# Kernel tuning notes

Measured on AMD Instinct MI355X. Metric: run time of the kernel, lower is better.

The kernel has to match this reference:

```python
import jax, jax.numpy as jnp
import numpy as np

B, S, D = 2, 2048, 1024
H, DH = 16, 64
EPS = 1e-5

def setup_inputs() -> dict:
    key = jax.random.key(0)
    ks = jax.random.split(key, 8)
    s = 0.02
    return {
        "x": jax.random.normal(ks[0], (B, S, D), dtype=jnp.float32),
        "ln_gamma": jnp.ones((D,), jnp.float32),
        "ln_beta": jnp.zeros((D,), jnp.float32),
        "wq": jax.random.normal(ks[1], (D, H * DH), jnp.float32) * s,
        "bq": jnp.zeros((H * DH,), jnp.float32),
        "wk": jax.random.normal(ks[2], (D, H * DH), jnp.float32) * s,
        "bk": jnp.zeros((H * DH,), jnp.float32),
        "wv": jax.random.normal(ks[3], (D, H * DH), jnp.float32) * s,
        "bv": jnp.zeros((H * DH,), jnp.float32),
        "wo": jax.random.normal(ks[4], (H * DH, D), jnp.float32) * s,
        "bo": jnp.zeros((D,), jnp.float32),
    }

def reference(x, ln_gamma, ln_beta, wq, bq, wk, bk, wv, bv, wo, bo):
    # Pre-LayerNorm over d_model
    mu = jnp.mean(x, axis=-1, keepdims=True)
    var = jnp.var(x, axis=-1, keepdims=True)
    xn = (x - mu) * jax.lax.rsqrt(var + EPS) * ln_gamma + ln_beta

    b, s, _ = xn.shape
    q = (xn @ wq + bq).reshape(b, s, H, DH)
    k = (xn @ wk + bk).reshape(b, s, H, DH)
    v = (xn @ wv + bv).reshape(b, s, H, DH)

    scale = jnp.sqrt(jnp.float32(DH))
    scores = jnp.einsum('bihd,bjhd->bhij', q, k) / scale  # [b,h,s,s]
    att = jax.nn.softmax(scores, axis=-1)
    out = jnp.einsum('bhij,bjhd->bihd', att, v).reshape(b, s, H * DH)
    return out @ wo + bo
```

## Files before the change

### kernel.cpp

```cpp
#include <hip/hip_runtime.h>
#include <math.h>

#define SEQ   2048
#define DM    1024
#define NHEAD 16
#define HD    64
#define NTOK  4096
#define EPS   1e-5f
#define SCALE_C 0.18033688f

typedef __attribute__((ext_vector_type(8))) short v8s;
typedef __attribute__((ext_vector_type(4))) short v4s;
typedef __attribute__((ext_vector_type(4))) float v4f;
typedef unsigned short ushort_t;

#define GLOAD16(g, l) __builtin_amdgcn_global_load_lds( \
    (const __attribute__((address_space(1))) unsigned int*)(g), \
    (__attribute__((address_space(3))) unsigned int*)(l), 16, 0, 0)

#if defined(__has_builtin)
#if __has_builtin(__builtin_amdgcn_mfma_f32_16x16x16_bf16)
#define MFMA16(va, vb, vc) __builtin_amdgcn_mfma_f32_16x16x16_bf16(va, vb, vc, 0, 0, 0)
#elif __has_builtin(__builtin_amdgcn_mfma_f32_16x16x16bf16_1k)
#define MFMA16(va, vb, vc) __builtin_amdgcn_mfma_f32_16x16x16bf16_1k(va, vb, vc, 0, 0, 0)
#endif
#endif
#ifndef MFMA16
__device__ __forceinline__ v4f mfma16_asm(v4s a, v4s b, v4f c) {
  asm volatile("s_nop 2\n\tv_mfma_f32_16x16x16_bf16 %0, %1, %2, %0\n\ts_nop 4"
               : "+v"(c) : "v"(a), "v"(b));
  return c;
}
#define MFMA16(va, vb, vc) mfma16_asm(va, vb, vc)
#endif

__device__ __forceinline__ unsigned short f2bf(float f) {
  union { float f; unsigned u; } v; v.f = f;
  unsigned r = v.u + 0x7FFFu + ((v.u >> 16) & 1u);
  return (unsigned short)(r >> 16);
}

__device__ __forceinline__ unsigned pack2_bf16(float a, float b) {
  union { float f; unsigned u; } ua, ub;
  ua.f = a; ub.f = b;
  return __builtin_amdgcn_perm(ub.u + 0x8000u, ua.u + 0x8000u, 0x07060302u);
}

__global__ __launch_bounds__(256) void ln_kernel(
    const float* __restrict__ x, const float* __restrict__ g,
    const float* __restrict__ be, ushort_t* __restrict__ y) {
  const int row = blockIdx.x;
  const int t = threadIdx.x;
  const float4 v = ((const float4*)(x + (size_t)row * DM))[t];
  float s  = v.x + v.y + v.z + v.w;
  float ss = v.x*v.x + v.y*v.y + v.z*v.z + v.w*v.w;
  #pragma unroll
  for (int off = 32; off > 0; off >>= 1) {
    s  += __shfl_down(s,  off, 64);
    ss += __shfl_down(ss, off, 64);
  }
  __shared__ float red[8];
  __shared__ float mu_s, rs_s;
  const int wid = t >> 6, lane = t & 63;
  if (lane == 0) { red[wid] = s; red[4 + wid] = ss; }
  __syncthreads();
  if (t == 0) {
    const float S  = red[0] + red[1] + red[2] + red[3];
    const float SS = red[4] + red[5] + red[6] + red[7];
    const float mu  = S * (1.0f / DM);
    const float var = SS * (1.0f / DM) - mu * mu;
    mu_s = mu; rs_s = rsqrtf(var + EPS);
  }
  __syncthreads();
  const float mu = mu_s, r = rs_s;
  const float4 gv = ((const float4*)g)[t];
  const float4 bv = ((const float4*)be)[t];
  ushort4 o;
  o.x = f2bf((v.x - mu) * r * gv.x + bv.x);
  o.y = f2bf((v.y - mu) * r * gv.y + bv.y);
  o.z = f2bf((v.z - mu) * r * gv.z + bv.z);
  o.w = f2bf((v.w - mu) * r * gv.w + bv.w);
  *(ushort4*)(y + (size_t)row * DM + t * 4) = o;
}

__global__ __launch_bounds__(256) void wt_kernel(
    const float* __restrict__ w0, const float* __restrict__ w1,
    const float* __restrict__ w2, const float* __restrict__ w3,
    ushort_t* __restrict__ o0, ushort_t* __restrict__ o1,
    ushort_t* __restrict__ o2, ushort_t* __restrict__ o3) {
  const int z = blockIdx.z;
  const float* w = (z==0) ? w0 : (z==1) ? w1 : (z==2) ? w2 : w3;
  ushort_t* o    = (z==0) ? o0 : (z==1) ? o1 : (z==2) ? o2 : o3;
  __shared__ float tile[64][65];
  const int t = threadIdx.x;
  const int n0 = blockIdx.x * 64, k0 = blockIdx.y * 64;
  const int r = t >> 4, c4 = (t & 15) * 4;
  #pragma unroll
  for (int i = 0; i < 4; ++i) {
    const float4 v = *(const float4*)(w + (size_t)(k0 + r + i*16) * DM + n0 + c4);
    tile[r + i*16][c4 + 0] = v.x;
    tile[r + i*16][c4 + 1] = v.y;
    tile[r + i*16][c4 + 2] = v.z;
    tile[r + i*16][c4 + 3] = v.w;
  }
  __syncthreads();
  #pragma unroll
  for (int i = 0; i < 4; ++i) {
    const int n = r + i*16;
    ushort4 o4;
    o4.x = f2bf(tile[c4 + 0][n]);
    o4.y = f2bf(tile[c4 + 1][n]);
    o4.z = f2bf(tile[c4 + 2][n]);
    o4.w = f2bf(tile[c4 + 3][n]);
    *(ushort4*)(o + (size_t)(n0 + n) * DM + k0 + c4) = o4;
  }
}

__device__ __forceinline__ void gemm_main(ushort_t* lsa, ushort_t* lsb,
    const ushort_t* A, const ushort_t* WT, int m0, int n0, v4f acc[4][4]) {
  const int tid = threadIdx.x;
  const int wid = tid >> 6, lane = tid & 63;
  const int mh = (wid & 1) << 6, nh = (wid >> 1) << 6;
  const int r16 = lane & 15, quad = lane >> 4;
  const int srow = lane >> 2, sch = lane & 3;
  for (int k0 = 0; k0 < DM; k0 += 32) {
    __syncthreads();
    #pragma unroll
    for (int j = 0; j < 2; ++j) {
      const int o = wid * 2 + j;
      GLOAD16(A  + (size_t)(m0 + o*16 + srow) * DM + k0 + sch*8, lsa + o*512);
      GLOAD16(WT + (size_t)(n0 + o*16 + srow) * DM + k0 + sch*8, lsb + o*512);
    }
    __syncthreads();
    v8s af[4], bfr[4];
    #pragma unroll
    for (int i = 0; i < 4; ++i) {
      af[i]  = *(const v8s*)(lsa + (mh + i*16 + r16)*32 + quad*8);
      bfr[i] = *(const v8s*)(lsb + (nh + i*16 + r16)*32 + quad*8);
    }
    #pragma unroll
    for (int i = 0; i < 4; ++i)
      #pragma unroll
      for (int j = 0; j < 4; ++j)
        acc[i][j] = __builtin_amdgcn_mfma_f32_16x16x32_bf16(af[i], bfr[j], acc[i][j], 0, 0, 0);
  }
}

__global__ __launch_bounds__(256, 2) void gemm_qkv(const ushort_t* __restrict__ xn,
    const ushort_t* __restrict__ wtq, const ushort_t* __restrict__ wtk, const ushort_t* __restrict__ wtv,
    const float* __restrict__ bq, const float* __restrict__ bk, const float* __restrict__ bv,
    ushort_t* __restrict__ qo, ushort_t* __restrict__ ko, ushort_t* __restrict__ vto) {
  __shared__ ushort_t lsa[128*32];
  __shared__ ushort_t lsb[128*32];
  const int z = blockIdx.z;
  const ushort_t* WT = (z == 0) ? wtq : (z == 1) ? wtk : wtv;
  const float* bias  = (z == 0) ? bq  : (z == 1) ? bk  : bv;
  const int m0 = blockIdx.y * 128, n0 = blockIdx.x * 128;
  v4f acc[4][4];
  #pragma unroll
  for (int i = 0; i < 4; ++i)
    #pragma unroll
    for (int j = 0; j < 4; ++j) acc[i][j] = (v4f){0.f, 0.f, 0.f, 0.f};
  gemm_main(lsa, lsb, xn, WT, m0, n0, acc);
  const int tid = threadIdx.x, wid = tid >> 6, lane = tid & 63;
  const int mh = (wid & 1) << 6, nh = (wid >> 1) << 6;
  const int r16 = lane & 15, quad = lane >> 4;
  if (z < 2) {
    ushort_t* out = (z == 0) ? qo : ko;
    const float sc = (z == 0) ? SCALE_C : 1.0f;
    #pragma unroll
    for (int bn = 0; bn < 4; ++bn) {
      const int col = n0 + nh + bn*16 + r16;
      const float bb = bias[col];
      #pragma unroll
      for (int am = 0; am < 4; ++am) {
        const int tb = m0 + mh + am*16 + quad*4;
        #pragma unroll
        for (int r = 0; r < 4; ++r)
          out[(size_t)(tb + r) * DM + col] = f2bf((acc[am][bn][r] + bb) * sc);
      }
    }
  } else {
    #pragma unroll
    for (int bn = 0; bn < 4; ++bn) {
      const int col = n0 + nh + bn*16 + r16;
      const float bb = bias[col];
      const int h = col >> 6, d = col & 63;
      #pragma unroll
      for (int am = 0; am < 4; ++am) {
        const int tb = m0 + mh + am*16 + quad*4;
        const int b = tb >> 11, t = tb & 2047;
        const int bh = b * NHEAD + h;
        ushort4 o4;
        o4.x = f2bf(acc[am][bn][0] + bb);
        o4.y = f2bf(acc[am][bn][1] + bb);
        o4.z = f2bf(acc[am][bn][2] + bb);
        o4.w = f2bf(acc[am][bn][3] + bb);
        const size_t idx = (size_t)bh * 131072 + (size_t)(t >> 6) * 4096 +
                           (size_t)((((t >> 4) & 3) * 4) + (d >> 4)) * 256 +
                           ((t >> 2) & 3) * 64 + (d & 15) * 4;
        *(ushort4*)(vto + idx) = o4;
      }
    }
  }
}

__global__ __launch_bounds__(256, 2) void gemm_out(const ushort_t* __restrict__ A,
    const ushort_t* __restrict__ WT, const float* __restrict__ bias,
    float* __restrict__ out) {
  __shared__ ushort_t lsa[128*32];
  __shared__ ushort_t lsb[128*32];
  const int m0 = blockIdx.y * 128, n0 = blockIdx.x * 128;
  v4f acc[4][4];
  #pragma unroll
  for (int i = 0; i < 4; ++i)
    #pragma unroll
    for (int j = 0; j < 4; ++j) acc[i][j] = (v4f){0.f, 0.f, 0.f, 0.f};
  gemm_main(lsa, lsb, A, WT, m0, n0, acc);
  const int tid = threadIdx.x, wid = tid >> 6, lane = tid & 63;
  const int mh = (wid & 1) << 6, nh = (wid >> 1) << 6;
  const int r16 = lane & 15, quad = lane >> 4;
  #pragma unroll
  for (int bn = 0; bn < 4; ++bn) {
    const int col = n0 + nh + bn*16 + r16;
    const float bb = bias[col];
    #pragma unroll
    for (int am = 0; am < 4; ++am) {
      const int tb = m0 + mh + am*16 + quad*4;
      #pragma unroll
      for (int r = 0; r < 4; ++r)
        out[(size_t)(tb + r) * DM + col] = acc[am][bn][r] + bb;
    }
  }
}

#define OHALF ((size_t)32 * 2048 * 64)
#define LHALF (32 * 2048)
template<int SPLIT>
__global__ __launch_bounds__(256, 8) void attn_kernel(
    const ushort_t* __restrict__ Q, const ushort_t* __restrict__ K,
    const ushort_t* __restrict__ Vt, ushort_t* __restrict__ O,
    float* __restrict__ Opart, float* __restrict__ lpart) {
  __shared__ ushort_t kbuf[8*512];
  __shared__ ushort_t vbuf[16*256];
  const int tid = threadIdx.x, wid = tid >> 6, lane = tid & 63;
  const int r16 = lane & 15, quad = lane >> 4;
  const int q0 = blockIdx.x * 64, bh = blockIdx.y;
  const int half = SPLIT ? blockIdx.z : 0;
  const int b = bh >> 4, h = bh & 15;
  const ushort_t* gQ = Q + (size_t)b * SEQ * DM + h * HD;
  const ushort_t* gK = K + (size_t)b * SEQ * DM + h * HD;
  const ushort_t* gV = Vt + (size_t)bh * 131072;

  const int qtok = q0 + wid * 16 + r16;
  const v8s qf0 = *(const v8s*)(gQ + (size_t)qtok * DM + quad * 8);
  const v8s qf1 = *(const v8s*)(gQ + (size_t)qtok * DM + 32 + quad * 8);
  v4f acco[4];
  #pragma unroll
  for (int i = 0; i < 4; ++i) acco[i] = (v4f){0.f, 0.f, 0.f, 0.f};
  float lrun = 0.f;

  const int NIT = SPLIT ? (SEQ / 128) : (SEQ / 64);
  const int kt0 = half * NIT;
  for (int it = 0; it < NIT; ++it) {
    const int kt = kt0 + it;
    const int k0 = kt * 64;
    __syncthreads();
    #pragma unroll
    for (int j = 0; j < 2; ++j) {
      const int o = wid * 2 + j;
      GLOAD16(gK + (size_t)(k0 + (o >> 1) * 16 + r16) * DM + (o & 1) * 32 + quad * 8,
              kbuf + o * 512);
    }
    #pragma unroll
    for (int j = 0; j < 2; ++j) {
      const int o = wid * 2 + j;
      GLOAD16(gV + (size_t)kt * 4096 + o * 512 + lane * 8, vbuf + o * 512);
    }
    __syncthreads();

    v4f sacc[4];
    #pragma unroll
    for (int g = 0; g < 4; ++g) sacc[g] = (v4f){0.f, 0.f, 0.f, 0.f};
    #pragma unroll
    for (int g = 0; g < 4; ++g) {
      const v8s ka0 = *(const v8s*)(kbuf + (g*2 + 0) * 512 + lane * 8);
      const v8s ka1 = *(const v8s*)(kbuf + (g*2 + 1) * 512 + lane * 8);
      sacc[g] = __builtin_amdgcn_mfma_f32_16x16x32_bf16(ka0, qf0, sacc[g], 0, 0, 0);
      sacc[g] = __builtin_amdgcn_mfma_f32_16x16x32_bf16(ka1, qf1, sacc[g], 0, 0, 0);
    }

    float ls = 0.f;
    v4s pfrag[4];
    #pragma unroll
    for (int g = 0; g < 4; ++g) {
      float e0 = __builtin_amdgcn_exp2f(sacc[g][0]);
      float e1 = __builtin_amdgcn_exp2f(sacc[g][1]);
      float e2 = __builtin_amdgcn_exp2f(sacc[g][2]);
      float e3 = __builtin_amdgcn_exp2f(sacc[g][3]);
      ls += (e0 + e1) + (e2 + e3);
      union { v4s s; uint2 u; } pk;
      pk.u.x = pack2_bf16(e0, e1);
      pk.u.y = pack2_bf16(e2, e3);
      pfrag[g] = pk.s;
    }
    ls += __shfl_xor(ls, 16, 64);
    ls += __shfl_xor(ls, 32, 64);
    lrun += ls;

    #pragma unroll
    for (int dg = 0; dg < 4; ++dg) {
      #pragma unroll
      for (int g = 0; g < 4; ++g) {
        const v4s vf = *(const v4s*)(vbuf + (g*4 + dg) * 256 + quad * 64 + r16 * 4);
        acco[dg] = MFMA16(vf, pfrag[g], acco[dg]);
      }
    }
  }

  if (SPLIT) {
    float* Op = Opart + half * OHALF + ((size_t)bh * SEQ + qtok) * 64;
    #pragma unroll
    for (int dg = 0; dg < 4; ++dg)
      *(v4f*)(Op + dg*16 + quad*4) = acco[dg];
    if (quad == 0) lpart[half * LHALF + bh * SEQ + qtok] = lrun;
  } else {
    const float inv = 1.f / lrun;
    ushort_t* gO = O + (size_t)b * SEQ * DM + h * HD;
    #pragma unroll
    for (int dg = 0; dg < 4; ++dg) {
      ushort4 o4;
      o4.x = f2bf(acco[dg][0] * inv);
      o4.y = f2bf(acco[dg][1] * inv);
      o4.z = f2bf(acco[dg][2] * inv);
      o4.w = f2bf(acco[dg][3] * inv);
      *(ushort4*)(gO + (size_t)qtok * DM + dg*16 + quad*4) = o4;
    }
  }
}

__global__ __launch_bounds__(256) void combine_kernel(
    const float* __restrict__ Opart, const float* __restrict__ lpart,
    ushort_t* __restrict__ ob) {
  const int tok = blockIdx.x;
  const int b = tok >> 11, t = tok & 2047;
  const int dm0 = threadIdx.x * 4;
  const int h = dm0 >> 6, d = dm0 & 63;
  const int bh = b * NHEAD + h;
  const size_t idx = ((size_t)bh * SEQ + t) * 64 + d;
  const float4 a = *(const float4*)(Opart + idx);
  const float4 c = *(const float4*)(Opart + OHALF + idx);
  const float l = lpart[bh * SEQ + t] + lpart[LHALF + bh * SEQ + t];
  const float inv = 1.f / l;
  ushort4 o4;
  o4.x = f2bf((a.x + c.x) * inv);
  o4.y = f2bf((a.y + c.y) * inv);
  o4.z = f2bf((a.z + c.z) * inv);
  o4.w = f2bf((a.w + c.w) * inv);
  *(ushort4*)(ob + (size_t)tok * DM + dm0) = o4;
}

extern "C" void kernel_launch(void* const* d_in, const int* in_sizes, int n_in,
                              void* d_out, int out_size, void* d_ws, size_t ws_size,
                              hipStream_t stream) {
  const float* x     = (const float*)d_in[0];
  const float* gamma = (const float*)d_in[1];
  const float* beta  = (const float*)d_in[2];
  const float* wq    = (const float*)d_in[3];
  const float* bq    = (const float*)d_in[4];
  const float* wk    = (const float*)d_in[5];
  const float* bk    = (const float*)d_in[6];
  const float* wv    = (const float*)d_in[7];
  const float* bv    = (const float*)d_in[8];
  const float* wo    = (const float*)d_in[9];
  const float* bo    = (const float*)d_in[10];
  float* out = (float*)d_out;

  unsigned char* w8 = (unsigned char*)d_ws;
  const size_t MB = 1024 * 1024;
  ushort_t* xn  = (ushort_t*)(w8 + 0 * MB);
  ushort_t* qb  = (ushort_t*)(w8 + 8 * MB);
  ushort_t* kb  = (ushort_t*)(w8 + 16 * MB);
  ushort_t* vt  = (ushort_t*)(w8 + 24 * MB);
  ushort_t* wtq = (ushort_t*)(w8 + 32 * MB);
  ushort_t* wtk = (ushort_t*)(w8 + 34 * MB);
  ushort_t* wtv = (ushort_t*)(w8 + 36 * MB);
  ushort_t* wto = (ushort_t*)(w8 + 38 * MB);
  float* Opart  = (float*)(w8 + 40 * MB);
  float* lpart  = (float*)(w8 + 72 * MB);
  ushort_t* ob  = xn;

  ln_kernel<<<dim3(NTOK), dim3(256), 0, stream>>>(x, gamma, beta, xn);
  wt_kernel<<<dim3(16, 16, 4), dim3(256), 0, stream>>>(wq, wk, wv, wo, wtq, wtk, wtv, wto);
  gemm_qkv<<<dim3(8, 32, 3), dim3(256), 0, stream>>>(xn, wtq, wtk, wtv, bq, bk, bv, qb, kb, vt);
  if (ws_size >= 73 * MB) {
    attn_kernel<1><<<dim3(SEQ / 64, 2 * NHEAD, 2), dim3(256), 0, stream>>>(
        qb, kb, vt, nullptr, Opart, lpart);
    combine_kernel<<<dim3(NTOK), dim3(256), 0, stream>>>(Opart, lpart, ob);
  } else {
    attn_kernel<0><<<dim3(SEQ / 64, 2 * NHEAD, 1), dim3(256), 0, stream>>>(
        qb, kb, vt, ob, nullptr, nullptr);
  }
  gemm_out<<<dim3(8, 32, 1), dim3(256), 0, stream>>>(ob, wto, bo, out);
}
```

Baseline: 217.7 us.

## Double-buffer K/V tiles in attention and merge layernorm with weight transpose

The attention kernel now keeps two LDS buffers for K and V and issues the global-to-LDS loads for the next tile before computing on the current one. This drops one barrier per iteration and lets memory traffic overlap the MFMA work. The layernorm and weight-transpose kernels are also merged into one launch, with block index choosing the role, which saves a launch and lets the two run side by side. The costs are doubled LDS per attention block, which may lower occupancy under the 8-block launch bound, and one extra redundant tile load on the last iteration.

Result: no change. 218.5 us (+0.4%).

```diff
diff --git a/kernel.cpp b/kernel.cpp
--- a/kernel.cpp
+++ b/kernel.cpp
@@ -46,73 +46,73 @@
   return __builtin_amdgcn_perm(ub.u + 0x8000u, ua.u + 0x8000u, 0x07060302u);
 }
 
-__global__ __launch_bounds__(256) void ln_kernel(
+__global__ __launch_bounds__(256) void prep_kernel(
     const float* __restrict__ x, const float* __restrict__ g,
-    const float* __restrict__ be, ushort_t* __restrict__ y) {
-  const int row = blockIdx.x;
-  const int t = threadIdx.x;
-  const float4 v = ((const float4*)(x + (size_t)row * DM))[t];
-  float s  = v.x + v.y + v.z + v.w;
-  float ss = v.x*v.x + v.y*v.y + v.z*v.z + v.w*v.w;
-  #pragma unroll
-  for (int off = 32; off > 0; off >>= 1) {
-    s  += __shfl_down(s,  off, 64);
-    ss += __shfl_down(ss, off, 64);
-  }
-  __shared__ float red[8];
-  __shared__ float mu_s, rs_s;
-  const int wid = t >> 6, lane = t & 63;
-  if (lane == 0) { red[wid] = s; red[4 + wid] = ss; }
-  __syncthreads();
-  if (t == 0) {
-    const float S  = red[0] + red[1] + red[2] + red[3];
-    const float SS = red[4] + red[5] + red[6] + red[7];
-    const float mu  = S * (1.0f / DM);
-    const float var = SS * (1.0f / DM) - mu * mu;
-    mu_s = mu; rs_s = rsqrtf(var + EPS);
-  }
-  __syncthreads();
-  const float mu = mu_s, r = rs_s;
-  const float4 gv = ((const float4*)g)[t];
-  const float4 bv = ((const float4*)be)[t];
-  ushort4 o;
-  o.x = f2bf((v.x - mu) * r * gv.x + bv.x);
-  o.y = f2bf((v.y - mu) * r * gv.y + bv.y);
-  o.z = f2bf((v.z - mu) * r * gv.z + bv.z);
-  o.w = f2bf((v.w - mu) * r * gv.w + bv.w);
-  *(ushort4*)(y + (size_t)row * DM + t * 4) = o;
-}
-
-__global__ __launch_bounds__(256) void wt_kernel(
+    const float* __restrict__ be, ushort_t* __restrict__ y,
     const float* __restrict__ w0, const float* __restrict__ w1,
     const float* __restrict__ w2, const float* __restrict__ w3,
     ushort_t* __restrict__ o0, ushort_t* __restrict__ o1,
     ushort_t* __restrict__ o2, ushort_t* __restrict__ o3) {
-  const int z = blockIdx.z;
-  const float* w = (z==0) ? w0 : (z==1) ? w1 : (z==2) ? w2 : w3;
-  ushort_t* o    = (z==0) ? o0 : (z==1) ? o1 : (z==2) ? o2 : o3;
+  __shared__ float red[8];
+  __shared__ float mu_s, rs_s;
   __shared__ float tile[64][65];
   const int t = threadIdx.x;
-  const int n0 = blockIdx.x * 64, k0 = blockIdx.y * 64;
-  const int r = t >> 4, c4 = (t & 15) * 4;
-  #pragma unroll
-  for (int i = 0; i < 4; ++i) {
-    const float4 v = *(const float4*)(w + (size_t)(k0 + r + i*16) * DM + n0 + c4);
-    tile[r + i*16][c4 + 0] = v.x;
-    tile[r + i*16][c4 + 1] = v.y;
-    tile[r + i*16][c4 + 2] = v.z;
-    tile[r + i*16][c4 + 3] = v.w;
-  }
-  __syncthreads();
-  #pragma unroll
-  for (int i = 0; i < 4; ++i) {
-    const int n = r + i*16;
-    ushort4 o4;
-    o4.x = f2bf(tile[c4 + 0][n]);
-    o4.y = f2bf(tile[c4 + 1][n]);
-    o4.z = f2bf(tile[c4 + 2][n]);
-    o4.w = f2bf(tile[c4 + 3][n]);
-    *(ushort4*)(o + (size_t)(n0 + n) * DM + k0 + c4) = o4;
+  if (blockIdx.x < NTOK) {
+    const int row = blockIdx.x;
+    const float4 v = ((const float4*)(x + (size_t)row * DM))[t];
+    float s  = v.x + v.y + v.z + v.w;
+    float ss = v.x*v.x + v.y*v.y + v.z*v.z + v.w*v.w;
+    #pragma unroll
+    for (int off = 32; off > 0; off >>= 1) {
+      s  += __shfl_down(s,  off, 64);
+      ss += __shfl_down(ss, off, 64);
+    }
+    const int wid = t >> 6, lane = t & 63;
+    if (lane == 0) { red[wid] = s; red[4 + wid] = ss; }
+    __syncthreads();
+    if (t == 0) {
+      const float S  = red[0] + red[1] + red[2] + red[3];
+      const float SS = red[4] + red[5] + red[6] + red[7];
+      const float mu  = S * (1.0f / DM);
+      const float var = SS * (1.0f / DM) - mu * mu;
+      mu_s = mu; rs_s = rsqrtf(var + EPS);
+    }
+    __syncthreads();
+    const float mu = mu_s, r = rs_s;
+    const float4 gv = ((const float4*)g)[t];
+    const float4 bv = ((const float4*)be)[t];
+    ushort4 o;
+    o.x = f2bf((v.x - mu) * r * gv.x + bv.x);
+    o.y = f2bf((v.y - mu) * r * gv.y + bv.y);
+    o.z = f2bf((v.z - mu) * r * gv.z + bv.z);
+    o.w = f2bf((v.w - mu) * r * gv.w + bv.w);
+    *(ushort4*)(y + (size_t)row * DM + t * 4) = o;
+  } else {
+    const int i = blockIdx.x - NTOK;
+    const int z = i >> 8;
+    const float* w = (z==0) ? w0 : (z==1) ? w1 : (z==2) ? w2 : w3;
+    ushort_t* o    = (z==0) ? o0 : (z==1) ? o1 : (z==2) ? o2 : o3;
+    const int n0 = (i & 15) * 64, k0 = ((i >> 4) & 15) * 64;
+    const int r = t >> 4, c4 = (t & 15) * 4;
+    #pragma unroll
+    for (int ii = 0; ii < 4; ++ii) {
+      const float4 v = *(const float4*)(w + (size_t)(k0 + r + ii*16) * DM + n0 + c4);
+      tile[r + ii*16][c4 + 0] = v.x;
+      tile[r + ii*16][c4 + 1] = v.y;
+      tile[r + ii*16][c4 + 2] = v.z;
+      tile[r + ii*16][c4 + 3] = v.w;
+    }
+    __syncthreads();
+    #pragma unroll
+    for (int ii = 0; ii < 4; ++ii) {
+      const int n = r + ii*16;
+      ushort4 o4;
+      o4.x = f2bf(tile[c4 + 0][n]);
+      o4.y = f2bf(tile[c4 + 1][n]);
+      o4.z = f2bf(tile[c4 + 2][n]);
+      o4.w = f2bf(tile[c4 + 3][n]);
+      *(ushort4*)(o + (size_t)(n0 + n) * DM + k0 + c4) = o4;
+    }
   }
 }
 
@@ -241,8 +241,8 @@
     const ushort_t* __restrict__ Q, const ushort_t* __restrict__ K,
     const ushort_t* __restrict__ Vt, ushort_t* __restrict__ O,
     float* __restrict__ Opart, float* __restrict__ lpart) {
-  __shared__ ushort_t kbuf[8*512];
-  __shared__ ushort_t vbuf[16*256];
+  __shared__ ushort_t kbuf[2][8*512];
+  __shared__ ushort_t vbuf[2][16*256];
   const int tid = threadIdx.x, wid = tid >> 6, lane = tid & 63;
   const int r16 = lane & 15, quad = lane >> 4;
   const int q0 = blockIdx.x * 64, bh = blockIdx.y;
@@ -262,30 +262,36 @@
 
   const int NIT = SPLIT ? (SEQ / 128) : (SEQ / 64);
   const int kt0 = half * NIT;
-  for (int it = 0; it < NIT; ++it) {
-    const int kt = kt0 + it;
+
+  auto stage = [&](int bs, int kt) {
     const int k0 = kt * 64;
-    __syncthreads();
     #pragma unroll
     for (int j = 0; j < 2; ++j) {
       const int o = wid * 2 + j;
       GLOAD16(gK + (size_t)(k0 + (o >> 1) * 16 + r16) * DM + (o & 1) * 32 + quad * 8,
-              kbuf + o * 512);
+              kbuf[bs] + o * 512);
     }
     #pragma unroll
     for (int j = 0; j < 2; ++j) {
       const int o = wid * 2 + j;
-      GLOAD16(gV + (size_t)kt * 4096 + o * 512 + lane * 8, vbuf + o * 512);
-    }
-    __syncthreads();
+      GLOAD16(gV + (size_t)kt * 4096 + o * 512 + lane * 8, vbuf[bs] + o * 512);
+    }
+  };
+
+  stage(0, kt0);
+  __syncthreads();
+
+  for (int it = 0; it < NIT; ++it) {
+    const int cur = it & 1;
+    stage(cur ^ 1, kt0 + ((it + 1 == NIT) ? 0 : it + 1));
 
     v4f sacc[4];
     #pragma unroll
     for (int g = 0; g < 4; ++g) sacc[g] = (v4f){0.f, 0.f, 0.f, 0.f};
     #pragma unroll
     for (int g = 0; g < 4; ++g) {
-      const v8s ka0 = *(const v8s*)(kbuf + (g*2 + 0) * 512 + lane * 8);
-      const v8s ka1 = *(const v8s*)(kbuf + (g*2 + 1) * 512 + lane * 8);
+      const v8s ka0 = *(const v8s*)(kbuf[cur] + (g*2 + 0) * 512 + lane * 8);
+      const v8s ka1 = *(const v8s*)(kbuf[cur] + (g*2 + 1) * 512 + lane * 8);
       sacc[g] = __builtin_amdgcn_mfma_f32_16x16x32_bf16(ka0, qf0, sacc[g], 0, 0, 0);
       sacc[g] = __builtin_amdgcn_mfma_f32_16x16x32_bf16(ka1, qf1, sacc[g], 0, 0, 0);
     }
@@ -312,10 +318,12 @@
     for (int dg = 0; dg < 4; ++dg) {
       #pragma unroll
       for (int g = 0; g < 4; ++g) {
-        const v4s vf = *(const v4s*)(vbuf + (g*4 + dg) * 256 + quad * 64 + r16 * 4);
+        const v4s vf = *(const v4s*)(vbuf[cur] + (g*4 + dg) * 256 + quad * 64 + r16 * 4);
         acco[dg] = MFMA16(vf, pfrag[g], acco[dg]);
       }
     }
+
+    __syncthreads();
   }
 
   if (SPLIT) {
@@ -390,8 +398,8 @@
   float* lpart  = (float*)(w8 + 72 * MB);
   ushort_t* ob  = xn;
 
-  ln_kernel<<<dim3(NTOK), dim3(256), 0, stream>>>(x, gamma, beta, xn);
-  wt_kernel<<<dim3(16, 16, 4), dim3(256), 0, stream>>>(wq, wk, wv, wo, wtq, wtk, wtv, wto);
+  prep_kernel<<<dim3(NTOK + 1024), dim3(256), 0, stream>>>(
+      x, gamma, beta, xn, wq, wk, wv, wo, wtq, wtk, wtv, wto);
   gemm_qkv<<<dim3(8, 32, 3), dim3(256), 0, stream>>>(xn, wtq, wtk, wtv, bq, bk, bv, qb, kb, vt);
   if (ws_size >= 73 * MB) {
     attn_kernel<1><<<dim3(SEQ / 64, 2 * NHEAD, 2), dim3(256), 0, stream>>>(
```
